# Kernel optimization log

Measured on AMD Instinct MI355X. Metric: run time of the kernel, lower is better.

The kernel has to match this reference:

```python
import jax, jax.numpy as jnp
import numpy as np

B, T, D, H, L = 64, 256, 64, 512, 10


def setup_inputs() -> dict:
    key = jax.random.key(0)
    ks = jax.random.split(key, 8)
    k_init = 1.0 / np.sqrt(H)  # PyTorch LSTMCell/Linear uniform init bound
    u = lambda k, shape: jax.random.uniform(k, shape, jnp.float32, -k_init, k_init)
    return {
        "x": jax.random.normal(ks[0], (B, T, D), jnp.float32),
        "W_ih0": u(ks[1], (4 * H, D)),        # layer 0 input weights
        "W_ih": u(ks[2], (L - 1, 4 * H, H)),  # layers 1..L-1 input weights
        "W_hh": u(ks[3], (L, 4 * H, H)),      # recurrent weights
        "b_ih": u(ks[4], (L, 4 * H)),
        "b_hh": u(ks[5], (L, 4 * H)),
        "W_out": u(ks[6], (D, H)),            # linear head weight
        "b_out": u(ks[7], (D,)),
    }


def _cell(x, h, c, W_i, W_h, b):
    # PyTorch LSTMCell: gates ordered (i, f, g, o)
    g = x @ W_i.T + h @ W_h.T + b  # [B, 4H]
    i, f, gg, o = jnp.split(g, 4, axis=-1)
    i = jax.nn.sigmoid(i)
    f = jax.nn.sigmoid(f)
    o = jax.nn.sigmoid(o)
    gg = jnp.tanh(gg)
    c_new = f * c + i * gg
    h_new = o * jnp.tanh(c_new)
    return h_new, c_new


def reference(x, W_ih0, W_ih, W_hh, b_ih, b_hh, W_out, b_out):
    b = b_ih + b_hh  # [L, 4H] — biases only ever appear summed

    def step(carry, x_t):
        h, c = carry  # each [L, B, H]
        h0, c0 = _cell(x_t, h[0], c[0], W_ih0, W_hh[0], b[0])
        hs, cs = [h0], [c0]
        for i in range(1, L):  # fixed small layer count
            hi, ci = _cell(hs[-1], h[i], c[i], W_ih[i - 1], W_hh[i], b[i])
            hs.append(hi)
            cs.append(ci)
        y = hs[-1] @ W_out.T + b_out  # [B, D] per-step linear head
        return (jnp.stack(hs), jnp.stack(cs)), y

    init = (jnp.zeros((L, B, H), jnp.float32), jnp.zeros((L, B, H), jnp.float32))
    _, ys = jax.lax.scan(step, init, jnp.swapaxes(x, 0, 1))  # ys: [T, B, D]
    return jnp.swapaxes(ys, 0, 1)  # [B, T, D]
```

## Files before the change

### kernel.cpp

```cpp
#include <hip/hip_runtime.h>
#include <hip/hip_fp16.h>
#include <stdint.h>

typedef _Float16 h8 __attribute__((ext_vector_type(8)));
typedef float f4 __attribute__((ext_vector_type(4)));

#define MFMA16(a,b,c) __builtin_amdgcn_mfma_f32_16x16x32_f16((a),(b),(c),0,0,0)

constexpr size_t XT_OFF = 0;
constexpr size_t XT_BYTES = 256ull * 4096 * 2;
constexpr size_t HL_OFF = XT_OFF + XT_BYTES;
constexpr size_t HL_BYTES = 10ull * 8 * 65536;
constexpr size_t HX_OFF = HL_OFF + HL_BYTES;
constexpr size_t HX_BYTES = 5ull * 8 * 65536;
constexpr size_t WSTRM_OFF = HX_OFF + HX_BYTES;
constexpr size_t WSTRM_BYTES = 144ull * 106496;
constexpr size_t PX_OFF = WSTRM_OFF + WSTRM_BYTES;
constexpr size_t CNT_OFF = PX_OFF + 1024;
constexpr size_t DIAG_OFF = CNT_OFF + 64;
constexpr size_t WS_NEED = DIAG_OFF + 64;

#define SCR 155648

__device__ __forceinline__ h8 gld16_p(const void* base, int voff) {
  h8 v; asm volatile("global_load_dwordx4 %0, %1, %2" : "=v"(v) : "v"(voff), "s"(base)); return v;
}
__device__ __forceinline__ h8 gld16_sc1(const void* base, int voff) {
  h8 v; asm volatile("global_load_dwordx4 %0, %1, %2 sc1" : "=v"(v) : "v"(voff), "s"(base)); return v;
}
__device__ __forceinline__ void gst16_sc1(const void* base, int voff, h8 v) {
  asm volatile("global_store_dwordx4 %0, %1, %2 sc1" :: "v"(voff), "v"(v), "s"(base) : "memory");
}
#define WAITI(n) do { asm volatile("s_waitcnt vmcnt(" #n ")" ::: "memory"); \
                      __builtin_amdgcn_sched_barrier(0); } while (0)

__device__ __forceinline__ int ld_prog(const int* p) {
  return __hip_atomic_load(p, __ATOMIC_RELAXED, __HIP_MEMORY_SCOPE_AGENT);
}
__device__ __forceinline__ void st_prog(int* p, int v) {
  __hip_atomic_store(p, v, __ATOMIC_RELAXED, __HIP_MEMORY_SCOPE_AGENT);
  __builtin_amdgcn_sched_barrier(0);
}
#define INV_L1() asm volatile("buffer_inv sc0\n\ts_waitcnt vmcnt(0)" ::: "memory")

__device__ __forceinline__ float sigm(float x) { return __fdividef(1.f, 1.f + __expf(-x)); }
__device__ __forceinline__ float tanh_f(float x) { return 1.f - __fdividef(2.f, __expf(2.f*x) + 1.f); }

__global__ __launch_bounds__(256) void zero_kernel(char* ws) {
  int i = blockIdx.x * 256 + threadIdx.x;
  if (i < 163840) {
    int layer = i >> 14, w = i & 16383;
    ((int*)(ws + HL_OFF))[(size_t)layer * 8 * 16384 + w] = 0;
  } else {
    int j = i - 163840;
    if (j < 168) ((int*)(ws + PX_OFF))[j] = -1;
    else if (j < 176) ((int*)(ws + CNT_OFF))[j - 168] = 0;
    else if (j == 176) ((int*)(ws + DIAG_OFF))[0] = 0;
  }
}

__global__ __launch_bounds__(256) void xprep_kernel(const float* __restrict__ X, char* ws) {
  int u = blockIdx.x * 256 + threadIdx.x;
  if (u >= 131072) return;
  int t = u >> 9, rem = u & 511, kg = rem >> 6, b = rem & 63;
  const float* src = X + ((size_t)b * 256 + t) * 64 + kg * 8;
  h8 v;
#pragma unroll
  for (int j = 0; j < 8; ++j) v[j] = (_Float16)src[j];
  *(h8*)(ws + XT_OFF + (size_t)u * 16) = v;
}

__global__ __launch_bounds__(256) void wsprep_kernel(const float* __restrict__ Wih,
                                                     const float* __restrict__ Whh, char* ws) {
  int u = blockIdx.x * 256 + threadIdx.x;
  if (u >= 144 * 6656) return;
  int cu = u / 6656, rem = u % 6656;
  int s = rem / 512, rem2 = rem % 512;
  int nt = rem2 >> 6, l = rem2 & 63;
  int ppc = l >> 2, lgc = l & 3;
  int L = 1 + cu / 16, cl = cu % 16, hbase = cl * 32;
  int kt = 4 + s, k = kt * 32 + lgc * 8;
  int row = (nt & 3) * 512 + hbase + ((nt >> 2) << 4) + ppc;
  const float* src = (k < 512) ? (Wih + (size_t)(L - 1) * 1048576 + (size_t)row * 512 + k)
                               : (Whh + (size_t)L * 1048576 + (size_t)row * 512 + (k - 512));
  h8 v;
#pragma unroll
  for (int j = 0; j < 8; ++j) v[j] = (_Float16)src[j];
  uint32_t off = (uint32_t)(ppc * 64 + lgc * 16) ^ (uint32_t)((ppc & 7) << 4);
  *(h8*)(ws + WSTRM_OFF + (size_t)cu * 106496 + (size_t)s * 8192 + (size_t)nt * 1024 + off) = v;
}

#define KTRES(r, Areg) do {                                                     \
  _Pragma("unroll") for (int nt_ = 0; nt_ < 8; ++nt_) {                         \
    h8 bv_ = *(const h8*)(lds + ((((r) * 8 + nt_) << 10) + swzo));              \
    acc[nt_] = MFMA16((Areg), bv_, acc[nt_]); } } while (0)

#define KTSTR(s, Areg) do {                                                     \
  _Pragma("unroll") for (int nt_ = 0; nt_ < 8; ++nt_)                           \
    acc[nt_] = MFMA16((Areg), Bst[s][nt_], acc[nt_]); } while (0)

#define ISSB(s) do { _Pragma("unroll") for (int nt_ = 0; nt_ < 8; ++nt_)        \
    Bst[s][nt_] = gld16_p(strm, (s) * 8192 + (nt_ << 10) + (int)swzo); } while (0)

#define ISSAS(i0) do { _Pragma("unroll") for (int i_ = 0; i_ < 4; ++i_)         \
    AS[(i0) + i_] = gld16_p(selb, ((i0) + i_) * 4096 + abb); } while (0)

__global__ __launch_bounds__(256, 1) void lstm_fused(
    const float* __restrict__ X, const float* __restrict__ Wih0,
    const float* __restrict__ Wih, const float* __restrict__ Whh,
    const float* __restrict__ bih, const float* __restrict__ bhh,
    const float* __restrict__ Wout, const float* __restrict__ bout,
    float* __restrict__ out, char* __restrict__ ws)
{
  extern __shared__ char lds[];
  const int tid = threadIdx.x;
  const int lane = tid & 63;
  const int wv = tid >> 6;
  const int pp = lane & 15;
  const int lg = lane >> 4;
  const int abb = lg * 1024 + (16 * wv + pp) * 16;
  const uint32_t swzo = (uint32_t)(pp * 64 + lg * 16) ^ (uint32_t)((pp & 7) << 4);

  int* progX = (int*)(ws + PX_OFF);
  int* diag  = (int*)(ws + DIAG_OFF);

  int xcd;
  asm volatile("s_getreg_b32 %0, hwreg(HW_REG_XCC_ID)" : "=s"(xcd));
  xcd &= 7;
  if (tid == 0) {
    int s = atomicAdd((int*)(ws + CNT_OFF) + xcd, 1);
    *(int*)lds = s;
  }
  __syncthreads();
  const int slot = *(int*)lds;
  __syncthreads();

  if (xcd == 5) {
    if (slot >= 8) return;
    const int hd = slot, d0 = hd * 8;
    const float* wrow0 = Wout + (size_t)(d0 + wv) * 512;
    const float* wrow1 = Wout + (size_t)(d0 + 4 + wv) * 512;
    const int b = lane;
    const bool pv = lane < 16;
    const int* pw = progX + 144 + (lane & 15);
    for (int th = 0; th < 256; ++th) {
      if (wv == 0) {
        int it = 0; bool bailed = false;
        for (;;) {
          int v = ld_prog(pw);
          if (__ballot(!pv || v >= th) == ~0ull) break;
          __builtin_amdgcn_s_sleep(1);
          if (++it > 60000) { bailed = true; break; }
        }
        if (bailed && lane == 0) atomicMax(diag, 10000 + th);
      }
      __builtin_amdgcn_s_barrier();
      const char* h9 = ws + HX_OFF + (size_t)(4 * 8 + ((th + 1) & 7)) * 65536;
      h8 H0[16], H1[16], H2[16], H3[16];
#pragma unroll
      for (int i = 0; i < 16; ++i) H0[i] = gld16_sc1(h9, i * 1024 + b * 16);
#pragma unroll
      for (int i = 0; i < 16; ++i) H1[i] = gld16_sc1(h9, (16 + i) * 1024 + b * 16);
      float a0 = bout[d0 + wv], a1 = bout[d0 + 4 + wv];
#define KH(kb, H) do { _Pragma("unroll") for (int i_ = 0; i_ < 16; ++i_) {      \
        h8 hv_ = H[i_]; float hf_[8];                                           \
        _Pragma("unroll") for (int j_ = 0; j_ < 8; ++j_) hf_[j_] = (float)hv_[j_]; \
        int kg_ = (kb) + i_;                                                    \
        f4 w0_ = *(const f4*)(wrow0 + kg_ * 8); f4 w1_ = *(const f4*)(wrow0 + kg_ * 8 + 4); \
        a0 += hf_[0]*w0_[0]+hf_[1]*w0_[1]+hf_[2]*w0_[2]+hf_[3]*w0_[3]           \
            + hf_[4]*w1_[0]+hf_[5]*w1_[1]+hf_[6]*w1_[2]+hf_[7]*w1_[3];          \
        f4 u0_ = *(const f4*)(wrow1 + kg_ * 8); f4 u1_ = *(const f4*)(wrow1 + kg_ * 8 + 4); \
        a1 += hf_[0]*u0_[0]+hf_[1]*u0_[1]+hf_[2]*u0_[2]+hf_[3]*u0_[3]           \
            + hf_[4]*u1_[0]+hf_[5]*u1_[1]+hf_[6]*u1_[2]+hf_[7]*u1_[3]; } } while (0)
      WAITI(16); KH(0, H0);
#pragma unroll
      for (int i = 0; i < 16; ++i) H2[i] = gld16_sc1(h9, (32 + i) * 1024 + b * 16);
      WAITI(16); KH(16, H1);
#pragma unroll
      for (int i = 0; i < 16; ++i) H3[i] = gld16_sc1(h9, (48 + i) * 1024 + b * 16);
      WAITI(16); KH(32, H2);
      WAITI(0);  KH(48, H3);
      out[(size_t)b * 16384 + (size_t)th * 64 + d0 + wv] = a0;
      out[(size_t)b * 16384 + (size_t)th * 64 + d0 + 4 + wv] = a1;
      __syncthreads();
      if (tid == 0) st_prog(progX + 160 + hd, th);
    }
    if (hd == 0 && tid == 0) {
      int dv = ld_prog(diag);
      if (dv != 0) out[0] = 1.0e6f + (float)dv;
    }
    return;
  }
  if (xcd > 5 || slot >= 32) return;

  const int L = 2 * xcd + (slot >= 16);
  const int cl = slot & 15;
  const int hbase = cl * 32;
  const bool oddL = (L & 1) != 0;

  if (L == 0) {
    for (int ch = tid; ch < 9216; ch += 256) {
      int r = ch >> 9, rem = ch & 511;
      int nt = rem >> 6, l = rem & 63, ppc = l >> 2, lgc = l & 3;
      int k = r * 32 + lgc * 8;
      int row = (nt & 3) * 512 + hbase + ((nt >> 2) << 4) + ppc;
      const float* src = (k < 64) ? (Wih0 + (size_t)row * 64 + k)
                                  : (Whh + (size_t)row * 512 + (k - 64));
      h8 v;
#pragma unroll
      for (int j = 0; j < 8; ++j) v[j] = (_Float16)src[j];
      uint32_t off = (uint32_t)(ppc * 64 + lgc * 16) ^ (uint32_t)((ppc & 7) << 4);
      *(h8*)(lds + ((r * 8 + nt) << 10) + off) = v;
    }
  } else {
    const float* WihL = Wih + (size_t)(L - 1) * 1048576;
    const float* WhhL = Whh + (size_t)L * 1048576;
    for (int ch = tid; ch < 9728; ch += 256) {
      int r = ch >> 9, rem = ch & 511;
      int nt = rem >> 6, l = rem & 63, ppc = l >> 2, lgc = l & 3;
      int rkt = r < 4 ? r : r + 13;
      int k = rkt * 32 + lgc * 8;
      int row = (nt & 3) * 512 + hbase + ((nt >> 2) << 4) + ppc;
      const float* src = (k < 512) ? (WihL + (size_t)row * 512 + k)
                                   : (WhhL + (size_t)row * 512 + (k - 512));
      h8 v;
#pragma unroll
      for (int j = 0; j < 8; ++j) v[j] = (_Float16)src[j];
      uint32_t off = (uint32_t)(ppc * 64 + lgc * 16) ^ (uint32_t)((ppc & 7) << 4);
      *(h8*)(lds + ((r * 8 + nt) << 10) + off) = v;
    }
  }
  float biasv[8];
#pragma unroll
  for (int nt = 0; nt < 8; ++nt) {
    int row = (nt & 3) * 512 + hbase + ((nt >> 2) << 4) + pp;
    biasv[nt] = bih[L * 2048 + row] + bhh[L * 2048 + row];
  }
  __syncthreads();

  const int jl = lane & 15;
  const int* pw = progX; bool pv = false; int dlt = 0;
  if (lane < 16)      { pv = true; pw = progX + L * 16 + jl; dlt = -1; }
  else if (lane < 32) { if (L > 0) { pv = true; pw = progX + (L - 1) * 16 + jl; dlt = 0; } }
  else if (lane < 48) {
    dlt = -7;
    if (L == 9) { if (jl < 8) { pv = true; pw = progX + 160 + jl; } }
    else        { pv = true; pw = progX + (L + 1) * 16 + jl; }
  }

  const char* hl = ws + HL_OFF;
  const char* hx = ws + HX_OFF;
  const char* strm = ws + WSTRM_OFF + (size_t)((L - 1) * 16 + cl) * 106496;
  const char* xt = ws + XT_OFF;

  float cv[2][4] = {{0,0,0,0},{0,0,0,0}};

  for (int t = 0; t < 256; ++t) {
    if (wv == 0) {
      int it = 0; bool bailed = false;
      for (;;) {
        int v = ld_prog(pw);
        if (__ballot(!pv || v >= t + dlt) == ~0ull) break;
        __builtin_amdgcn_s_sleep(1);
        if (++it > 60000) { bailed = true; break; }
      }
      if (bailed && lane == 0) atomicMax(diag, L * 1000 + t);
      INV_L1();
    }
    __builtin_amdgcn_s_barrier();

    f4 acc[8];
#pragma unroll
    for (int j = 0; j < 8; ++j) acc[j] = (f4){0.f, 0.f, 0.f, 0.f};

    if (L == 0) {
      const char* selb = hl + (size_t)(t & 7) * 65536;
      h8 X0 = gld16_p(xt, t * 8192 + abb);
      h8 X1 = gld16_p(xt, t * 8192 + 4096 + abb);
      h8 AS[16];
#pragma unroll
      for (int i = 0; i < 16; ++i) AS[i] = gld16_p(selb, i * 4096 + abb);
      WAITI(17); KTRES(0, X0);
      WAITI(16); KTRES(1, X1);
      WAITI(15); KTRES(2, AS[0]);  WAITI(14); KTRES(3, AS[1]);
      WAITI(13); KTRES(4, AS[2]);  WAITI(12); KTRES(5, AS[3]);
      WAITI(11); KTRES(6, AS[4]);  WAITI(10); KTRES(7, AS[5]);
      WAITI(9);  KTRES(8, AS[6]);  WAITI(8);  KTRES(9, AS[7]);
      WAITI(7);  KTRES(10, AS[8]); WAITI(6);  KTRES(11, AS[9]);
      WAITI(5);  KTRES(12, AS[10]); WAITI(4); KTRES(13, AS[11]);
      WAITI(3);  KTRES(14, AS[12]); WAITI(2); KTRES(15, AS[13]);
      WAITI(1);  KTRES(16, AS[14]); WAITI(0); KTRES(17, AS[15]);
    } else {
      const char* botb = oddL ? (hl + (size_t)((L - 1) * 8 + ((t + 1) & 7)) * 65536)
                              : (hx + (size_t)(((L - 1) >> 1) * 8 + ((t + 1) & 7)) * 65536);
      const char* selb = hl + (size_t)(L * 8 + (t & 7)) * 65536;
      h8 AB[16], AS[16], Bst[13][8];
      if (oddL) {
#pragma unroll
        for (int i = 0; i < 16; ++i) AB[i] = gld16_p(botb, i * 4096 + abb);
      } else {
#pragma unroll
        for (int i = 0; i < 16; ++i) AB[i] = gld16_sc1(botb, i * 4096 + abb);
      }
      ISSB(0); ISSB(1);
      WAITI(31); KTRES(0, AB[0]); ISSB(2);
      WAITI(38); KTRES(1, AB[1]); ISSB(3);
      WAITI(45); KTRES(2, AB[2]); ISSB(4);
      WAITI(52); KTRES(3, AB[3]); ISSB(5);
      WAITI(40); KTSTR(0, AB[4]); ISSB(6);
      WAITI(40); KTSTR(1, AB[5]); ISSB(7);
      WAITI(40); KTSTR(2, AB[6]); ISSB(8);
      WAITI(40); KTSTR(3, AB[7]); ISSB(9);
      WAITI(40); KTSTR(4, AB[8]); ISSB(10);
      WAITI(40); KTSTR(5, AB[9]); ISSB(11);
      WAITI(40); KTSTR(6, AB[10]); ISSB(12);
      WAITI(40); KTSTR(7, AB[11]); ISSAS(0);
      WAITI(36); KTSTR(8, AB[12]); ISSAS(4);
      WAITI(28); KTSTR(9, AB[13]); ISSAS(8);
      WAITI(20); KTSTR(10, AB[14]); ISSAS(12);
      WAITI(12); KTSTR(11, AB[15]);
      WAITI(4);  KTSTR(12, AS[0]);
      KTRES(4, AS[1]);  KTRES(5, AS[2]);  KTRES(6, AS[3]);
      KTRES(7, AS[4]);  KTRES(8, AS[5]);  KTRES(9, AS[6]);
      KTRES(10, AS[7]); KTRES(11, AS[8]); KTRES(12, AS[9]);
      KTRES(13, AS[10]); KTRES(14, AS[11]);
      WAITI(3); KTRES(15, AS[12]);
      WAITI(2); KTRES(16, AS[13]);
      WAITI(1); KTRES(17, AS[14]);
      WAITI(0); KTRES(18, AS[15]);
    }

    const int brow = 16 * wv + 4 * lg;
#pragma unroll
    for (int jh = 0; jh < 2; ++jh) {
      const int hgl = jh * 16 + pp;
#pragma unroll
      for (int r = 0; r < 4; ++r) {
        float gi = sigm(acc[4*jh+0][r] + biasv[4*jh+0]);
        float gf = sigm(acc[4*jh+1][r] + biasv[4*jh+1]);
        float gg = tanh_f(acc[4*jh+2][r] + biasv[4*jh+2]);
        float go = sigm(acc[4*jh+3][r] + biasv[4*jh+3]);
        float cc = gf * cv[jh][r] + gi * gg;
        cv[jh][r] = cc;
        float hh = go * tanh_f(cc);
        *(_Float16*)(lds + SCR + ((hgl >> 3) << 10) + (brow + r) * 16 + ((hgl & 7) << 1))
            = (_Float16)hh;
      }
    }
    __syncthreads();
    {
      const int kg_l = tid >> 6, b = tid & 63;
      h8 vv = *(const h8*)(lds + SCR + tid * 16);
      const int goff = (((hbase >> 3) + kg_l) << 10) + b * 16;
      char* HdL = (char*)(hl + (size_t)(L * 8 + ((t + 1) & 7)) * 65536);
      *(h8*)(HdL + goff) = vv;
      if (oddL) {
        const char* HdX = hx + (size_t)((L >> 1) * 8 + ((t + 1) & 7)) * 65536;
        gst16_sc1(HdX, goff, vv);
      }
    }
    asm volatile("s_waitcnt vmcnt(0)" ::: "memory");
    __syncthreads();
    if (tid == 0) st_prog(progX + L * 16 + cl, t);
  }
}

extern "C" void kernel_launch(void* const* d_in, const int* in_sizes, int n_in,
                              void* d_out, int out_size, void* d_ws, size_t ws_size,
                              hipStream_t stream) {
  const float* X    = (const float*)d_in[0];
  const float* Wih0 = (const float*)d_in[1];
  const float* Wih  = (const float*)d_in[2];
  const float* Whh  = (const float*)d_in[3];
  const float* bihp = (const float*)d_in[4];
  const float* bhhp = (const float*)d_in[5];
  const float* Wout = (const float*)d_in[6];
  const float* bout = (const float*)d_in[7];
  float* out = (float*)d_out;
  char* ws = (char*)d_ws;
  (void)in_sizes; (void)n_in; (void)out_size;
  if (ws_size < WS_NEED) return;

  hipFuncSetAttribute((const void*)lstm_fused,
                      hipFuncAttributeMaxDynamicSharedMemorySize, 163840);

  zero_kernel<<<642, 256, 0, stream>>>(ws);
  xprep_kernel<<<512, 256, 0, stream>>>(X, ws);
  wsprep_kernel<<<3744, 256, 0, stream>>>(Wih, Whh, ws);
  lstm_fused<<<256, 256, 163840, stream>>>(X, Wih0, Wih, Whh, bihp, bhhp,
                                           Wout, bout, out, ws);
}
```

Before: 2.895 ms.

## Split progress flags per locality and deepen hidden-state ring buffer

Adds a second progress-flag array (progL) written with plain volatile stores and read after an L1 invalidate, used for same-XCD producer/consumer pairs, while cross-XCD dependencies keep the agent-scope atomic flags. The hidden-state ring buffer depth becomes a runtime parameter (16 when workspace allows, else 8), loosening the anti-dependency slack so producers can run further ahead. The polling loop now spins a few times before sleeping. The aim is lower inter-block synchronization latency in the wavefront-pipelined LSTM, at the cost of more workspace and reliance on cache coherence behaviour of non-atomic flags.

After: 2.942 ms. About the same (+1.6%).

```diff
diff --git a/kernel.cpp b/kernel.cpp
--- a/kernel.cpp
+++ b/kernel.cpp
@@ -9,18 +9,13 @@
 
 constexpr size_t XT_OFF = 0;
 constexpr size_t XT_BYTES = 256ull * 4096 * 2;
-constexpr size_t HL_OFF = XT_OFF + XT_BYTES;
-constexpr size_t HL_BYTES = 10ull * 8 * 65536;
-constexpr size_t HX_OFF = HL_OFF + HL_BYTES;
-constexpr size_t HX_BYTES = 5ull * 8 * 65536;
-constexpr size_t WSTRM_OFF = HX_OFF + HX_BYTES;
+constexpr size_t WSTRM_OFF = XT_OFF + XT_BYTES;
 constexpr size_t WSTRM_BYTES = 144ull * 106496;
-constexpr size_t PX_OFF = WSTRM_OFF + WSTRM_BYTES;
+constexpr size_t PL_OFF = WSTRM_OFF + WSTRM_BYTES;
+constexpr size_t PX_OFF = PL_OFF + 1024;
 constexpr size_t CNT_OFF = PX_OFF + 1024;
 constexpr size_t DIAG_OFF = CNT_OFF + 64;
-constexpr size_t WS_NEED = DIAG_OFF + 64;
-
-#define SCR 155648
+constexpr size_t HL_OFF = DIAG_OFF + 4032;
 
 __device__ __forceinline__ h8 gld16_p(const void* base, int voff) {
   h8 v; asm volatile("global_load_dwordx4 %0, %1, %2" : "=v"(v) : "v"(voff), "s"(base)); return v;
@@ -28,6 +23,9 @@
 __device__ __forceinline__ h8 gld16_sc1(const void* base, int voff) {
   h8 v; asm volatile("global_load_dwordx4 %0, %1, %2 sc1" : "=v"(v) : "v"(voff), "s"(base)); return v;
 }
+__device__ __forceinline__ void gst16_p(const void* base, int voff, h8 v) {
+  asm volatile("global_store_dwordx4 %0, %1, %2" :: "v"(voff), "v"(v), "s"(base) : "memory");
+}
 __device__ __forceinline__ void gst16_sc1(const void* base, int voff, h8 v) {
   asm volatile("global_store_dwordx4 %0, %1, %2 sc1" :: "v"(voff), "v"(v), "s"(base) : "memory");
 }
@@ -37,25 +35,22 @@
 __device__ __forceinline__ int ld_prog(const int* p) {
   return __hip_atomic_load(p, __ATOMIC_RELAXED, __HIP_MEMORY_SCOPE_AGENT);
 }
-__device__ __forceinline__ void st_prog(int* p, int v) {
-  __hip_atomic_store(p, v, __ATOMIC_RELAXED, __HIP_MEMORY_SCOPE_AGENT);
-  __builtin_amdgcn_sched_barrier(0);
-}
 #define INV_L1() asm volatile("buffer_inv sc0\n\ts_waitcnt vmcnt(0)" ::: "memory")
 
 __device__ __forceinline__ float sigm(float x) { return __fdividef(1.f, 1.f + __expf(-x)); }
 __device__ __forceinline__ float tanh_f(float x) { return 1.f - __fdividef(2.f, __expf(2.f*x) + 1.f); }
 
-__global__ __launch_bounds__(256) void zero_kernel(char* ws) {
+__global__ __launch_bounds__(256) void zero_kernel(char* ws, int rs) {
   int i = blockIdx.x * 256 + threadIdx.x;
   if (i < 163840) {
     int layer = i >> 14, w = i & 16383;
-    ((int*)(ws + HL_OFF))[(size_t)layer * 8 * 16384 + w] = 0;
+    ((int*)(ws + HL_OFF))[(size_t)layer * rs * 16384 + w] = 0;
   } else {
     int j = i - 163840;
-    if (j < 168) ((int*)(ws + PX_OFF))[j] = -1;
-    else if (j < 176) ((int*)(ws + CNT_OFF))[j - 168] = 0;
-    else if (j == 176) ((int*)(ws + DIAG_OFF))[0] = 0;
+    if (j < 168) ((int*)(ws + PL_OFF))[j] = -1;
+    else if (j < 336) ((int*)(ws + PX_OFF))[j - 168] = -1;
+    else if (j < 344) ((int*)(ws + CNT_OFF))[j - 336] = 0;
+    else if (j == 344) ((int*)(ws + DIAG_OFF))[0] = 0;
   }
 }
 
@@ -105,12 +100,14 @@
 #define ISSAS(i0) do { _Pragma("unroll") for (int i_ = 0; i_ < 4; ++i_)         \
     AS[(i0) + i_] = gld16_p(selb, ((i0) + i_) * 4096 + abb); } while (0)
 
+#define SCR 155648
+
 __global__ __launch_bounds__(256, 1) void lstm_fused(
     const float* __restrict__ X, const float* __restrict__ Wih0,
     const float* __restrict__ Wih, const float* __restrict__ Whh,
     const float* __restrict__ bih, const float* __restrict__ bhh,
     const float* __restrict__ Wout, const float* __restrict__ bout,
-    float* __restrict__ out, char* __restrict__ ws)
+    float* __restrict__ out, char* __restrict__ ws, int rs)
 {
   extern __shared__ char lds[];
   const int tid = threadIdx.x;
@@ -120,9 +117,13 @@
   const int lg = lane >> 4;
   const int abb = lg * 1024 + (16 * wv + pp) * 16;
   const uint32_t swzo = (uint32_t)(pp * 64 + lg * 16) ^ (uint32_t)((pp & 7) << 4);
-
+  const int rsm = rs - 1;
+
+  int* progL = (int*)(ws + PL_OFF);
   int* progX = (int*)(ws + PX_OFF);
   int* diag  = (int*)(ws + DIAG_OFF);
+  const char* hl = ws + HL_OFF;
+  const char* hx = hl + (size_t)10 * rs * 65536;
 
   int xcd;
   asm volatile("s_getreg_b32 %0, hwreg(HW_REG_XCC_ID)" : "=s"(xcd));
@@ -155,7 +156,7 @@
         if (bailed && lane == 0) atomicMax(diag, 10000 + th);
       }
       __builtin_amdgcn_s_barrier();
-      const char* h9 = ws + HX_OFF + (size_t)(4 * 8 + ((th + 1) & 7)) * 65536;
+      const char* h9 = hx + (size_t)(4 * rs + ((th + 1) & rsm)) * 65536;
       h8 H0[16], H1[16], H2[16], H3[16];
 #pragma unroll
       for (int i = 0; i < 16; ++i) H0[i] = gld16_sc1(h9, i * 1024 + b * 16);
@@ -183,7 +184,8 @@
       out[(size_t)b * 16384 + (size_t)th * 64 + d0 + wv] = a0;
       out[(size_t)b * 16384 + (size_t)th * 64 + d0 + 4 + wv] = a1;
       __syncthreads();
-      if (tid == 0) st_prog(progX + 160 + hd, th);
+      if (tid == 0)
+        __hip_atomic_store(progX + 160 + hd, th, __ATOMIC_RELAXED, __HIP_MEMORY_SCOPE_AGENT);
     }
     if (hd == 0 && tid == 0) {
       int dv = ld_prog(diag);
@@ -239,17 +241,22 @@
   __syncthreads();
 
   const int jl = lane & 15;
-  const int* pw = progX; bool pv = false; int dlt = 0;
-  if (lane < 16)      { pv = true; pw = progX + L * 16 + jl; dlt = -1; }
-  else if (lane < 32) { if (L > 0) { pv = true; pw = progX + (L - 1) * 16 + jl; dlt = 0; } }
-  else if (lane < 48) {
-    dlt = -7;
-    if (L == 9) { if (jl < 8) { pv = true; pw = progX + 160 + jl; } }
-    else        { pv = true; pw = progX + (L + 1) * 16 + jl; }
-  }
-
-  const char* hl = ws + HL_OFF;
-  const char* hx = ws + HX_OFF;
+  bool okL = false, okX = false;
+  int ixL = 0, ixX = 0, dL = 0, dX = 0;
+  if (lane < 16) { okL = true; ixL = L * 16 + jl; dL = -1; }
+  else if (lane < 32) {
+    if (L > 0) {
+      if (oddL) { okL = true; ixL = (L - 1) * 16 + jl; dL = 0; }
+      else      { okX = true; ixX = (L - 1) * 16 + jl; dX = 0; }
+    }
+  } else if (lane < 48) {
+    if (L == 9)    { if (jl < 8) { okX = true; ixX = 160 + jl; dX = -rsm; } }
+    else if (oddL) { okX = true; ixX = (L + 1) * 16 + jl; dX = -rsm; }
+    else           { okL = true; ixL = (L + 1) * 16 + jl; dL = -rsm; }
+  }
+  const volatile int* aL = (const volatile int*)(progL + ixL);
+  const int* aX = progX + ixX;
+
   const char* strm = ws + WSTRM_OFF + (size_t)((L - 1) * 16 + cl) * 106496;
   const char* xt = ws + XT_OFF;
 
@@ -259,13 +266,15 @@
     if (wv == 0) {
       int it = 0; bool bailed = false;
       for (;;) {
-        int v = ld_prog(pw);
-        if (__ballot(!pv || v >= t + dlt) == ~0ull) break;
-        __builtin_amdgcn_s_sleep(1);
+        INV_L1();
+        int vL = *aL;
+        int vX = ld_prog(aX);
+        bool ok = (!okL || vL >= t + dL) && (!okX || vX >= t + dX);
+        if (__ballot(ok) == ~0ull) break;
         if (++it > 60000) { bailed = true; break; }
+        if (it > 4) __builtin_amdgcn_s_sleep(1);
       }
       if (bailed && lane == 0) atomicMax(diag, L * 1000 + t);
-      INV_L1();
     }
     __builtin_amdgcn_s_barrier();
 
@@ -274,7 +283,7 @@
     for (int j = 0; j < 8; ++j) acc[j] = (f4){0.f, 0.f, 0.f, 0.f};
 
     if (L == 0) {
-      const char* selb = hl + (size_t)(t & 7) * 65536;
+      const char* selb = hl + (size_t)(t & rsm) * 65536;
       h8 X0 = gld16_p(xt, t * 8192 + abb);
       h8 X1 = gld16_p(xt, t * 8192 + 4096 + abb);
       h8 AS[16];
@@ -291,9 +300,9 @@
       WAITI(3);  KTRES(14, AS[12]); WAITI(2); KTRES(15, AS[13]);
       WAITI(1);  KTRES(16, AS[14]); WAITI(0); KTRES(17, AS[15]);
     } else {
-      const char* botb = oddL ? (hl + (size_t)((L - 1) * 8 + ((t + 1) & 7)) * 65536)
-                              : (hx + (size_t)(((L - 1) >> 1) * 8 + ((t + 1) & 7)) * 65536);
-      const char* selb = hl + (size_t)(L * 8 + (t & 7)) * 65536;
+      const char* botb = oddL ? (hl + (size_t)((L - 1) * rs + ((t + 1) & rsm)) * 65536)
+                              : (hx + (size_t)(((L - 1) >> 1) * rs + ((t + 1) & rsm)) * 65536);
+      const char* selb = hl + (size_t)(L * rs + (t & rsm)) * 65536;
       h8 AB[16], AS[16], Bst[13][8];
       if (oddL) {
 #pragma unroll
@@ -352,16 +361,20 @@
       const int kg_l = tid >> 6, b = tid & 63;
       h8 vv = *(const h8*)(lds + SCR + tid * 16);
       const int goff = (((hbase >> 3) + kg_l) << 10) + b * 16;
-      char* HdL = (char*)(hl + (size_t)(L * 8 + ((t + 1) & 7)) * 65536);
-      *(h8*)(HdL + goff) = vv;
+      const char* HdL = hl + (size_t)(L * rs + ((t + 1) & rsm)) * 65536;
+      gst16_p(HdL, goff, vv);
       if (oddL) {
-        const char* HdX = hx + (size_t)((L >> 1) * 8 + ((t + 1) & 7)) * 65536;
+        const char* HdX = hx + (size_t)((L >> 1) * rs + ((t + 1) & rsm)) * 65536;
         gst16_sc1(HdX, goff, vv);
       }
     }
     asm volatile("s_waitcnt vmcnt(0)" ::: "memory");
     __syncthreads();
-    if (tid == 0) st_prog(progX + L * 16 + cl, t);
+    if (tid == 0) {
+      *(volatile int*)(progL + L * 16 + cl) = t;
+      __hip_atomic_store(progX + L * 16 + cl, t,
+                         __ATOMIC_RELAXED, __HIP_MEMORY_SCOPE_AGENT);
+    }
   }
 }
 
@@ -379,14 +392,18 @@
   float* out = (float*)d_out;
   char* ws = (char*)d_ws;
   (void)in_sizes; (void)n_in; (void)out_size;
-  if (ws_size < WS_NEED) return;
+
+  int rs = 16;
+  size_t need = HL_OFF + 15ull * rs * 65536;
+  if (ws_size < need) { rs = 8; need = HL_OFF + 15ull * rs * 65536; }
+  if (ws_size < need) return;
 
   hipFuncSetAttribute((const void*)lstm_fused,
                       hipFuncAttributeMaxDynamicSharedMemorySize, 163840);
 
-  zero_kernel<<<642, 256, 0, stream>>>(ws);
+  zero_kernel<<<642, 256, 0, stream>>>(ws, rs);
   xprep_kernel<<<512, 256, 0, stream>>>(X, ws);
   wsprep_kernel<<<3744, 256, 0, stream>>>(Wih, Whh, ws);
   lstm_fused<<<256, 256, 163840, stream>>>(X, Wih0, Wih, Whh, bihp, bhhp,
-                                           Wout, bout, out, ws);
-}
+                                           Wout, bout, out, ws, rs);
+}
```
